# Kernel tuning notes

Measured on AMD Instinct MI355X. Metric: run time of the kernel, lower is better.

## Reference

```python
import jax, jax.numpy as jnp
import numpy as np

NE = 200000   # num_entities
NR = 16       # num_relations
D  = 128      # embed_dim
B  = 4096     # batch
S  = 64       # neighbors per node
L  = 2        # num_layers
H  = 4        # attention heads (hardcoded in module)


def _ln(x, g, b, eps=1e-5):
    m = jnp.mean(x, -1, keepdims=True)
    v = jnp.mean((x - m) ** 2, -1, keepdims=True)
    return (x - m) * jax.lax.rsqrt(v + eps) * g + b


def setup_inputs() -> dict:
    key = jax.random.key(0)
    ks = jax.random.split(key, 12)
    s = 0.05
    return {
        'drug_entity_indices': jax.random.randint(ks[0], (B,), 0, NE),
        'adj_entity': jax.random.randint(ks[1], (B, S), 0, NE),
        'adj_relation': jax.random.randint(ks[2], (B, S), 0, NR),
        'edge_weights': jax.random.uniform(ks[3], (B, S), dtype=jnp.float32),
        'entity_emb': jax.random.normal(ks[4], (NE, D), jnp.float32) * s,
        'W_rgcn': jax.random.normal(ks[5], (L, NR, D, D), jnp.float32) * s,
        'res_w': jax.random.normal(ks[6], (L, D, D), jnp.float32) * s,
        'res_b': jnp.zeros((L, D), jnp.float32),
        'proj_w': jax.random.normal(ks[7], (L, D, D), jnp.float32) * s,
        'proj_b': jnp.zeros((L, D), jnp.float32),
        'ln_g': jnp.ones((L, D), jnp.float32),
        'ln_b': jnp.zeros((L, D), jnp.float32),
        'in_proj_w': jax.random.normal(ks[8], (3 * D, D), jnp.float32) * s,
        'in_proj_b': jnp.zeros((3 * D,), jnp.float32),
        'out_proj_w': jax.random.normal(ks[9], (D, D), jnp.float32) * s,
        'out_proj_b': jnp.zeros((D,), jnp.float32),
        'fln_g': jnp.ones((D,), jnp.float32),
        'fln_b': jnp.zeros((D,), jnp.float32),
    }


def reference(drug_entity_indices, adj_entity, adj_relation, edge_weights,
              entity_emb, W_rgcn, res_w, res_b, proj_w, proj_b, ln_g, ln_b,
              in_proj_w, in_proj_b, out_proj_w, out_proj_b, fln_g, fln_b):
    node = entity_emb[drug_entity_indices]           # [B,D] combined_emb
    nbr = entity_emb[adj_entity]                     # [B,S,D]
    # Route each edge to its relation: sum_s nbr*ew*[rel==r] then one GEMM per relation
    # (mathematically identical to the per-relation masked matmul loop in torch).
    onehot = jax.nn.one_hot(adj_relation, NR, dtype=node.dtype)      # [B,S,R]
    pre = jnp.einsum('bsd,bsr->brd', nbr * edge_weights[..., None], onehot)
    outs = []
    for l in range(L):
        msgs = jnp.einsum('brd,rde->be', pre, W_rgcn[l])             # [B,D]
        h = jax.nn.relu(node + msgs + node @ res_w[l].T + res_b[l])  # RGCNAggregator
        node = _ln(h @ proj_w[l].T + proj_b[l] + node, ln_g[l], ln_b[l])
        outs.append(node)
    x = jnp.stack(outs, 0)                           # [L,B,D] seq-first
    qkv = x @ in_proj_w.T + in_proj_b
    q, k, v = jnp.split(qkv, 3, axis=-1)
    hd = D // H
    def heads(t):
        return t.reshape(L, B, H, hd).transpose(1, 2, 0, 3)          # [B,H,L,hd]
    q, k, v = heads(q), heads(k), heads(v)
    att = jax.nn.softmax(jnp.einsum('bhld,bhmd->bhlm', q, k) / np.sqrt(hd).astype(np.float32), axis=-1)
    o = jnp.einsum('bhlm,bhmd->bhld', att, v).transpose(2, 0, 1, 3).reshape(L, B, D)
    o = o @ out_proj_w.T + out_proj_b
    return _ln(o.mean(0), fln_g, fln_b)              # [B,D]
```

## Files before the change

### kernel.cpp

```cpp
#include <hip/hip_runtime.h>
#include <math.h>

#define NRREL 16
#define DDIM 128
#define BBATCH 4096
#define SNBR 64

typedef __attribute__((ext_vector_type(8))) short short8;
typedef __attribute__((ext_vector_type(4))) float floatx4;

__device__ __forceinline__ unsigned short f2bf(float f) {
    unsigned u = __builtin_bit_cast(unsigned, f);
    u += 0x7fffu + ((u >> 16) & 1u);
    return (unsigned short)(u >> 16);
}
__device__ __forceinline__ float bf2f(unsigned short u) {
    return __builtin_bit_cast(float, ((unsigned)u) << 16);
}

__device__ __forceinline__ void gl_lds16(const unsigned short* g, unsigned short* l) {
    __builtin_amdgcn_global_load_lds(
        (const __attribute__((address_space(1))) void*)g,
        (__attribute__((address_space(3))) void*)l, 16, 0, 0);
}

extern "C" __global__ __launch_bounds__(256)
void k_front(const int* __restrict__ drug, const int* __restrict__ adj_e,
             const int* __restrict__ adj_r, const float* __restrict__ ew,
             const float* __restrict__ emb, const float* __restrict__ W_rgcn,
             const float* __restrict__ res_w, const float* __restrict__ proj_w,
             const float* __restrict__ in_w, const float* __restrict__ out_w,
             unsigned short* __restrict__ pre_bf, float* __restrict__ node_f,
             unsigned short* __restrict__ Wcat, unsigned short* __restrict__ resw,
             unsigned short* __restrict__ projw, unsigned short* __restrict__ inw,
             unsigned short* __restrict__ outw)
{
    __shared__ union {
        struct {
            int memb[16][64];
            int cnt[16];
            int sent[64];
            float swt[64];
        } g;
        struct { float tileT[64 * 65]; } w;
    } sm;

    const int bid = blockIdx.x, t = threadIdx.x;

    if (bid < BBATCH) {
        const int b = bid;
        if (t < 16) sm.g.cnt[t] = 0;
        __syncthreads();
        if (t < 64) {
            sm.g.sent[t] = adj_e[b * SNBR + t];
            sm.g.swt[t]  = ew[b * SNBR + t];
            int r = adj_r[b * SNBR + t];
            int slot = atomicAdd(&sm.g.cnt[r], 1);
            sm.g.memb[r][slot] = t;
        }
        if (t >= 64 && t < 96) {
            int tt = t - 64;
            float4 nf = *(const float4*)(emb + (size_t)drug[b] * DDIM + 4 * tt);
            *(float4*)(node_f + (size_t)b * DDIM + 4 * tt) = nf;
        }
        __syncthreads();
        const int r = t >> 4, g8 = t & 15;
        const int n = sm.g.cnt[r];
        float acc[8] = {0.f, 0.f, 0.f, 0.f, 0.f, 0.f, 0.f, 0.f};
        if (n > 0) {
            int s = sm.g.memb[r][0];
            float wq = sm.g.swt[s];
            const float* p = emb + (size_t)sm.g.sent[s] * DDIM + 8 * g8;
            float4 v0 = *(const float4*)p;
            float4 v1 = *(const float4*)(p + 4);
            for (int j = 1; j < n; ++j) {
                int s2 = sm.g.memb[r][j];
                float wq2 = sm.g.swt[s2];
                const float* p2 = emb + (size_t)sm.g.sent[s2] * DDIM + 8 * g8;
                float4 u0 = *(const float4*)p2;
                float4 u1 = *(const float4*)(p2 + 4);
                acc[0] = fmaf(v0.x, wq, acc[0]); acc[1] = fmaf(v0.y, wq, acc[1]);
                acc[2] = fmaf(v0.z, wq, acc[2]); acc[3] = fmaf(v0.w, wq, acc[3]);
                acc[4] = fmaf(v1.x, wq, acc[4]); acc[5] = fmaf(v1.y, wq, acc[5]);
                acc[6] = fmaf(v1.z, wq, acc[6]); acc[7] = fmaf(v1.w, wq, acc[7]);
                v0 = u0; v1 = u1; wq = wq2;
            }
            acc[0] = fmaf(v0.x, wq, acc[0]); acc[1] = fmaf(v0.y, wq, acc[1]);
            acc[2] = fmaf(v0.z, wq, acc[2]); acc[3] = fmaf(v0.w, wq, acc[3]);
            acc[4] = fmaf(v1.x, wq, acc[4]); acc[5] = fmaf(v1.y, wq, acc[5]);
            acc[6] = fmaf(v1.z, wq, acc[6]); acc[7] = fmaf(v1.w, wq, acc[7]);
        }
        short8 o;
        #pragma unroll
        for (int jj = 0; jj < 8; ++jj) o[jj] = (short)f2bf(acc[jj]);
        *(short8*)(pre_bf + (size_t)b * 2048 + r * DDIM + 8 * g8) = o;
    } else if (bid < BBATCH + 128) {
        const int bid2 = bid - BBATCH;
        const int l = bid2 >> 6, rem = bid2 & 63;
        const int k0 = (rem >> 1) * 64, e0 = (rem & 1) * 64;
        #pragma unroll
        for (int i = 0; i < 4; ++i) {
            int flat = t + 256 * i;
            int k = flat >> 4, c = flat & 15;
            float4 v = *(const float4*)(W_rgcn + ((size_t)(l * 2048 + k0 + k)) * 128 + e0 + 4 * c);
            sm.w.tileT[(4 * c + 0) * 65 + k] = v.x;
            sm.w.tileT[(4 * c + 1) * 65 + k] = v.y;
            sm.w.tileT[(4 * c + 2) * 65 + k] = v.z;
            sm.w.tileT[(4 * c + 3) * 65 + k] = v.w;
        }
        __syncthreads();
        const int e = t >> 2, m = t & 3;
        #pragma unroll
        for (int half = 0; half < 2; ++half) {
            int kk = 16 * m + 8 * half;
            short8 o;
            #pragma unroll
            for (int j = 0; j < 8; ++j) o[j] = (short)f2bf(sm.w.tileT[e * 65 + kk + j]);
            *(short8*)(Wcat + ((size_t)(l * 128 + e0 + e)) * 2048 + k0 + kk) = o;
        }
    } else {
        int j4 = ((bid - BBATCH - 128) * 256 + t) * 4;
        const float* src; unsigned short* dst; int off;
        if (j4 < 32768)       { src = res_w;  dst = resw;  off = j4; }
        else if (j4 < 65536)  { src = proj_w; dst = projw; off = j4 - 32768; }
        else if (j4 < 114688) { src = in_w;   dst = inw;   off = j4 - 65536; }
        else                  { src = out_w;  dst = outw;  off = j4 - 114688; }
        float4 v = *(const float4*)(src + off);
        ushort4 o = { f2bf(v.x), f2bf(v.y), f2bf(v.z), f2bf(v.w) };
        *(ushort4*)(dst + off) = o;
    }
}

extern "C" __global__ __launch_bounds__(512)
void k_tail(const unsigned short* __restrict__ pre_bf, const unsigned short* __restrict__ Wcat,
            const float* __restrict__ node_fg,
            const unsigned short* __restrict__ resw, const unsigned short* __restrict__ projw,
            const float* __restrict__ res_b, const float* __restrict__ proj_b,
            const float* __restrict__ ln_g, const float* __restrict__ ln_b,
            const unsigned short* __restrict__ inw, const float* __restrict__ in_b,
            const unsigned short* __restrict__ outw, const float* __restrict__ out_b,
            const float* __restrict__ fg, const float* __restrict__ fb,
            float* __restrict__ outp)
{
    __shared__ union {
        struct { unsigned short preA[16 * 2056]; } a;
        struct {
            unsigned short h_b16[16 * 136];
            unsigned short xs_l[32 * 136];
            unsigned short qkvl[32 * 392];
        } t;
    } sm;
    __shared__ float node_ln[16 * 132];
    __shared__ unsigned short node_b16[16 * 136];
    __shared__ float msum[16 * 260];
    __shared__ float psum[8][16], psq[8][16];

    const int t = threadIdx.x, w = t >> 6, lane = t & 63, l15 = lane & 15, q = lane >> 4;
    const int r0 = blockIdx.x * 16;

    #pragma unroll
    for (int i = 0; i < 8; ++i) {
        int row = 2 * w + (i & 1), chunk = i >> 1;
        gl_lds16(pre_bf + (size_t)(r0 + row) * 2048 + chunk * 512 + 8 * lane,
                 sm.a.preA + row * 2056 + chunk * 512);
    }
    {
        int rr = t >> 5, c = t & 31;
        float4 v = *(const float4*)(node_fg + (size_t)(r0 + rr) * DDIM + 4 * c);
        *(float4*)(node_ln + rr * 132 + 4 * c) = v;
        ushort4 o = { f2bf(v.x), f2bf(v.y), f2bf(v.z), f2bf(v.w) };
        *(ushort4*)(node_b16 + rr * 136 + 4 * c) = o;
    }
    __syncthreads();

    {
        floatx4 macc[2] = {};
        const unsigned short* ap = sm.a.preA + l15 * 2056 + 8 * q;
        const unsigned short* bp = Wcat + (size_t)(32 * w + l15) * 2048 + 8 * q;
        #pragma unroll 8
        for (int k = 0; k < 2048; k += 32) {
            short8 A = *(const short8*)(ap + k);
            #pragma unroll
            for (int ni = 0; ni < 2; ++ni) {
                short8 B = *(const short8*)(bp + (size_t)(ni * 16) * 2048 + k);
                macc[ni] = __builtin_amdgcn_mfma_f32_16x16x32_bf16(A, B, macc[ni], 0, 0, 0);
            }
        }
        #pragma unroll
        for (int ni = 0; ni < 2; ++ni) {
            int gc = 32 * w + ni * 16 + l15;
            #pragma unroll
            for (int r = 0; r < 4; ++r)
                msum[(4 * q + r) * 260 + gc] = macc[ni][r];
        }
    }
    __syncthreads();

    for (int l = 0; l < 2; ++l) {
        {
            const unsigned short* Bw = resw + (size_t)l * DDIM * DDIM;
            floatx4 acc = {};
            const unsigned short* ap = node_b16 + l15 * 136 + 8 * q;
            #pragma unroll
            for (int kk = 0; kk < DDIM; kk += 32) {
                short8 A = *(const short8*)(ap + kk);
                short8 B = *(const short8*)(Bw + (size_t)(16 * w + l15) * DDIM + kk + 8 * q);
                acc = __builtin_amdgcn_mfma_f32_16x16x32_bf16(A, B, acc, 0, 0, 0);
            }
            int gc = 16 * w + l15;
            float rb = res_b[l * DDIM + gc];
            #pragma unroll
            for (int r = 0; r < 4; ++r) {
                int lr = 4 * q + r;
                float v = acc[r] + rb + node_ln[lr * 132 + gc] + msum[lr * 260 + l * DDIM + gc];
                sm.t.h_b16[lr * 136 + gc] = f2bf(v > 0.f ? v : 0.f);
            }
        }
        __syncthreads();
        {
            const unsigned short* Bw = projw + (size_t)l * DDIM * DDIM;
            floatx4 acc = {};
            const unsigned short* ap = sm.t.h_b16 + l15 * 136 + 8 * q;
            #pragma unroll
            for (int kk = 0; kk < DDIM; kk += 32) {
                short8 A = *(const short8*)(ap + kk);
                short8 B = *(const short8*)(Bw + (size_t)(16 * w + l15) * DDIM + kk + 8 * q);
                acc = __builtin_amdgcn_mfma_f32_16x16x32_bf16(A, B, acc, 0, 0, 0);
            }
            int gc = 16 * w + l15;
            float vv[4];
            float s4[4] = {0, 0, 0, 0}, sq4[4] = {0, 0, 0, 0};
            float pb = proj_b[l * DDIM + gc];
            #pragma unroll
            for (int r = 0; r < 4; ++r) {
                int lr = 4 * q + r;
                float v = acc[r] + pb + node_ln[lr * 132 + gc];
                vv[r] = v; s4[r] += v; sq4[r] += v * v;
            }
            #pragma unroll
            for (int r = 0; r < 4; ++r)
                #pragma unroll
                for (int off2 = 8; off2 >= 1; off2 >>= 1) {
                    s4[r] += __shfl_xor(s4[r], off2, 64);
                    sq4[r] += __shfl_xor(sq4[r], off2, 64);
                }
            if (l15 == 0) {
                #pragma unroll
                for (int r = 0; r < 4; ++r) {
                    psum[w][4 * q + r] = s4[r];
                    psq[w][4 * q + r] = sq4[r];
                }
            }
            __syncthreads();
            float g2 = ln_g[l * DDIM + gc], bb = ln_b[l * DDIM + gc];
            #pragma unroll
            for (int r = 0; r < 4; ++r) {
                int lr = 4 * q + r;
                float ssum = 0.f, ssq = 0.f;
                #pragma unroll
                for (int ww = 0; ww < 8; ++ww) { ssum += psum[ww][lr]; ssq += psq[ww][lr]; }
                float mean = ssum * (1.f / DDIM);
                float var = ssq * (1.f / DDIM) - mean * mean;
                float val = (vv[r] - mean) * rsqrtf(var + 1e-5f) * g2 + bb;
                node_ln[lr * 132 + gc] = val;
                unsigned short ub = f2bf(val);
                node_b16[lr * 136 + gc] = ub;
                sm.t.xs_l[(2 * lr + l) * 136 + gc] = ub;
            }
            __syncthreads();
        }
    }

    {
        floatx4 acc[6] = {};
        const unsigned short* ap = sm.t.xs_l + (16 * (w & 1) + l15) * 136 + 8 * q;
        #pragma unroll
        for (int kk = 0; kk < DDIM; kk += 32) {
            short8 A = *(const short8*)(ap + kk);
            #pragma unroll
            for (int ni = 0; ni < 6; ++ni) {
                short8 B = *(const short8*)(inw + (size_t)(96 * (w >> 1) + ni * 16 + l15) * DDIM + kk + 8 * q);
                acc[ni] = __builtin_amdgcn_mfma_f32_16x16x32_bf16(A, B, acc[ni], 0, 0, 0);
            }
        }
        #pragma unroll
        for (int ni = 0; ni < 6; ++ni) {
            int gc = 96 * (w >> 1) + ni * 16 + l15;
            float ib = in_b[gc];
            #pragma unroll
            for (int r = 0; r < 4; ++r)
                sm.t.qkvl[(16 * (w & 1) + 4 * q + r) * 392 + gc] = f2bf(acc[ni][r] + ib);
        }
    }
    __syncthreads();

    if (t < 128) {
        int g4 = t >> 3, j = t & 7;
        const unsigned short* row0 = sm.t.qkvl + (2 * g4) * 392;
        const unsigned short* row1 = row0 + 392;
        float p00 = 0.f, p01 = 0.f, p10 = 0.f, p11 = 0.f;
        #pragma unroll
        for (int dd = 0; dd < 16; ++dd) {
            int d = 16 * j + dd;
            float q0 = bf2f(row0[d]), k0 = bf2f(row0[128 + d]);
            float q1 = bf2f(row1[d]), k1 = bf2f(row1[128 + d]);
            p00 = fmaf(q0, k0, p00); p01 = fmaf(q0, k1, p01);
            p10 = fmaf(q1, k0, p10); p11 = fmaf(q1, k1, p11);
        }
        p00 += __shfl_xor(p00, 1, 64); p01 += __shfl_xor(p01, 1, 64);
        p10 += __shfl_xor(p10, 1, 64); p11 += __shfl_xor(p11, 1, 64);
        const float sc = 0.17677669529663687f;
        p00 *= sc; p01 *= sc; p10 *= sc; p11 *= sc;
        float m0 = fmaxf(p00, p01), e00 = expf(p00 - m0), e01 = expf(p01 - m0);
        float i0 = 1.f / (e00 + e01);
        float m1 = fmaxf(p10, p11), e10 = expf(p10 - m1), e11 = expf(p11 - m1);
        float i1 = 1.f / (e10 + e11);
        #pragma unroll
        for (int dd = 0; dd < 16; ++dd) {
            int d = 16 * j + dd;
            float v0 = bf2f(row0[256 + d]), v1 = bf2f(row1[256 + d]);
            sm.t.xs_l[(2 * g4) * 136 + d]     = f2bf((e00 * v0 + e01 * v1) * i0);
            sm.t.xs_l[(2 * g4 + 1) * 136 + d] = f2bf((e10 * v0 + e11 * v1) * i1);
        }
    }
    __syncthreads();

    {
        floatx4 acc[2] = {};
        const unsigned short* ap = sm.t.xs_l + (16 * (w & 1) + l15) * 136 + 8 * q;
        #pragma unroll
        for (int kk = 0; kk < DDIM; kk += 32) {
            short8 A = *(const short8*)(ap + kk);
            #pragma unroll
            for (int ni = 0; ni < 2; ++ni) {
                short8 B = *(const short8*)(outw + (size_t)(32 * (w >> 1) + ni * 16 + l15) * DDIM + kk + 8 * q);
                acc[ni] = __builtin_amdgcn_mfma_f32_16x16x32_bf16(A, B, acc[ni], 0, 0, 0);
            }
        }
        float av[2][2];
        float s2[2] = {0, 0}, sq2[2] = {0, 0};
        #pragma unroll
        for (int ni = 0; ni < 2; ++ni) {
            int gc = 32 * (w >> 1) + ni * 16 + l15;
            float ob = out_b[gc];
            #pragma unroll
            for (int rr = 0; rr < 2; ++rr) {
                float v = 0.5f * (acc[ni][2 * rr] + acc[ni][2 * rr + 1]) + ob;
                av[ni][rr] = v; s2[rr] += v; sq2[rr] += v * v;
            }
        }
        #pragma unroll
        for (int rr = 0; rr < 2; ++rr)
            #pragma unroll
            for (int off2 = 8; off2 >= 1; off2 >>= 1) {
                s2[rr] += __shfl_xor(s2[rr], off2, 64);
                sq2[rr] += __shfl_xor(sq2[rr], off2, 64);
            }
        if (l15 == 0) {
            #pragma unroll
            for (int rr = 0; rr < 2; ++rr) {
                psum[w][2 * q + rr] = s2[rr];
                psq[w][2 * q + rr] = sq2[rr];
            }
        }
        __syncthreads();
        #pragma unroll
        for (int ni = 0; ni < 2; ++ni) {
            int gc = 32 * (w >> 1) + ni * 16 + l15;
            float g2 = fg[gc], bb = fb[gc];
            #pragma unroll
            for (int rr = 0; rr < 2; ++rr) {
                int idx = 2 * q + rr;
                int bl = 8 * (w & 1) + idx;
                float ssum = psum[w & 1][idx] + psum[(w & 1) + 2][idx]
                           + psum[(w & 1) + 4][idx] + psum[(w & 1) + 6][idx];
                float ssq  = psq[w & 1][idx] + psq[(w & 1) + 2][idx]
                           + psq[(w & 1) + 4][idx] + psq[(w & 1) + 6][idx];
                float mean = ssum * (1.f / DDIM);
                float var = ssq * (1.f / DDIM) - mean * mean;
                outp[(size_t)(r0 + bl) * DDIM + gc] = (av[ni][rr] - mean) * rsqrtf(var + 1e-5f) * g2 + bb;
            }
        }
    }
}

extern "C" void kernel_launch(void* const* d_in, const int* in_sizes, int n_in,
                              void* d_out, int out_size, void* d_ws, size_t ws_size,
                              hipStream_t stream) {
    const int*   drug_idx = (const int*)d_in[0];
    const int*   adj_ent  = (const int*)d_in[1];
    const int*   adj_rel  = (const int*)d_in[2];
    const float* ew       = (const float*)d_in[3];
    const float* emb      = (const float*)d_in[4];
    const float* W_rgcn   = (const float*)d_in[5];
    const float* res_w    = (const float*)d_in[6];
    const float* res_b    = (const float*)d_in[7];
    const float* proj_w   = (const float*)d_in[8];
    const float* proj_b   = (const float*)d_in[9];
    const float* ln_g     = (const float*)d_in[10];
    const float* ln_b     = (const float*)d_in[11];
    const float* in_w     = (const float*)d_in[12];
    const float* in_b     = (const float*)d_in[13];
    const float* out_w    = (const float*)d_in[14];
    const float* out_b    = (const float*)d_in[15];
    const float* fg       = (const float*)d_in[16];
    const float* fb       = (const float*)d_in[17];
    float* outp = (float*)d_out;

    char* ws = (char*)d_ws;
    size_t off = 0;
    auto alloc = [&](size_t bytes) { size_t o = off; off = (off + bytes + 255) & ~(size_t)255; return o; };
    unsigned short* pre_bf  = (unsigned short*)(ws + alloc((size_t)BBATCH * 2048 * 2));
    float*          node_f  = (float*)         (ws + alloc((size_t)BBATCH * 128 * 4));
    unsigned short* Wcat    = (unsigned short*)(ws + alloc((size_t)256 * 2048 * 2));
    unsigned short* resw    = (unsigned short*)(ws + alloc((size_t)2 * 128 * 128 * 2));
    unsigned short* projw   = (unsigned short*)(ws + alloc((size_t)2 * 128 * 128 * 2));
    unsigned short* inw     = (unsigned short*)(ws + alloc((size_t)384 * 128 * 2));
    unsigned short* outw    = (unsigned short*)(ws + alloc((size_t)128 * 128 * 2));

    hipLaunchKernelGGL(k_front, dim3(BBATCH + 256), dim3(256), 0, stream,
                       drug_idx, adj_ent, adj_rel, ew, emb, W_rgcn,
                       res_w, proj_w, in_w, out_w,
                       pre_bf, node_f, Wcat, resw, projw, inw, outw);
    hipLaunchKernelGGL(k_tail, dim3(256), dim3(512), 0, stream,
                       pre_bf, Wcat, node_f, resw, projw, res_b, proj_b, ln_g, ln_b,
                       inw, in_b, outw, out_b, fg, fb, outp);
}
```

Measured before the change: 240.6 us.

## Fuse neighbor gather and relation binning into the tail kernel

Moves the per-relation weighted neighbor aggregation from the front kernel into the main tail kernel, which now writes pre-activations straight into LDS. This removes the bf16 pre buffer (16 MB) and node buffer round trip through global memory. The front kernel keeps only weight conversion. The gather now runs on only 256 blocks instead of 4096, which lowers the parallelism available to hide the latency of the random embedding loads.

```diff
diff --git a/kernel.cpp b/kernel.cpp
--- a/kernel.cpp
+++ b/kernel.cpp
@@ -18,95 +18,29 @@
     return __builtin_bit_cast(float, ((unsigned)u) << 16);
 }
 
-__device__ __forceinline__ void gl_lds16(const unsigned short* g, unsigned short* l) {
-    __builtin_amdgcn_global_load_lds(
-        (const __attribute__((address_space(1))) void*)g,
-        (__attribute__((address_space(3))) void*)l, 16, 0, 0);
-}
-
 extern "C" __global__ __launch_bounds__(256)
-void k_front(const int* __restrict__ drug, const int* __restrict__ adj_e,
-             const int* __restrict__ adj_r, const float* __restrict__ ew,
-             const float* __restrict__ emb, const float* __restrict__ W_rgcn,
-             const float* __restrict__ res_w, const float* __restrict__ proj_w,
-             const float* __restrict__ in_w, const float* __restrict__ out_w,
-             unsigned short* __restrict__ pre_bf, float* __restrict__ node_f,
-             unsigned short* __restrict__ Wcat, unsigned short* __restrict__ resw,
-             unsigned short* __restrict__ projw, unsigned short* __restrict__ inw,
-             unsigned short* __restrict__ outw)
+void k_prep(const float* __restrict__ W_rgcn,
+            const float* __restrict__ res_w, const float* __restrict__ proj_w,
+            const float* __restrict__ in_w, const float* __restrict__ out_w,
+            unsigned short* __restrict__ Wcat, unsigned short* __restrict__ resw,
+            unsigned short* __restrict__ projw, unsigned short* __restrict__ inw,
+            unsigned short* __restrict__ outw)
 {
-    __shared__ union {
-        struct {
-            int memb[16][64];
-            int cnt[16];
-            int sent[64];
-            float swt[64];
-        } g;
-        struct { float tileT[64 * 65]; } w;
-    } sm;
-
+    __shared__ float tileT[64 * 65];
     const int bid = blockIdx.x, t = threadIdx.x;
 
-    if (bid < BBATCH) {
-        const int b = bid;
-        if (t < 16) sm.g.cnt[t] = 0;
-        __syncthreads();
-        if (t < 64) {
-            sm.g.sent[t] = adj_e[b * SNBR + t];
-            sm.g.swt[t]  = ew[b * SNBR + t];
-            int r = adj_r[b * SNBR + t];
-            int slot = atomicAdd(&sm.g.cnt[r], 1);
-            sm.g.memb[r][slot] = t;
-        }
-        if (t >= 64 && t < 96) {
-            int tt = t - 64;
-            float4 nf = *(const float4*)(emb + (size_t)drug[b] * DDIM + 4 * tt);
-            *(float4*)(node_f + (size_t)b * DDIM + 4 * tt) = nf;
-        }
-        __syncthreads();
-        const int r = t >> 4, g8 = t & 15;
-        const int n = sm.g.cnt[r];
-        float acc[8] = {0.f, 0.f, 0.f, 0.f, 0.f, 0.f, 0.f, 0.f};
-        if (n > 0) {
-            int s = sm.g.memb[r][0];
-            float wq = sm.g.swt[s];
-            const float* p = emb + (size_t)sm.g.sent[s] * DDIM + 8 * g8;
-            float4 v0 = *(const float4*)p;
-            float4 v1 = *(const float4*)(p + 4);
-            for (int j = 1; j < n; ++j) {
-                int s2 = sm.g.memb[r][j];
-                float wq2 = sm.g.swt[s2];
-                const float* p2 = emb + (size_t)sm.g.sent[s2] * DDIM + 8 * g8;
-                float4 u0 = *(const float4*)p2;
-                float4 u1 = *(const float4*)(p2 + 4);
-                acc[0] = fmaf(v0.x, wq, acc[0]); acc[1] = fmaf(v0.y, wq, acc[1]);
-                acc[2] = fmaf(v0.z, wq, acc[2]); acc[3] = fmaf(v0.w, wq, acc[3]);
-                acc[4] = fmaf(v1.x, wq, acc[4]); acc[5] = fmaf(v1.y, wq, acc[5]);
-                acc[6] = fmaf(v1.z, wq, acc[6]); acc[7] = fmaf(v1.w, wq, acc[7]);
-                v0 = u0; v1 = u1; wq = wq2;
-            }
-            acc[0] = fmaf(v0.x, wq, acc[0]); acc[1] = fmaf(v0.y, wq, acc[1]);
-            acc[2] = fmaf(v0.z, wq, acc[2]); acc[3] = fmaf(v0.w, wq, acc[3]);
-            acc[4] = fmaf(v1.x, wq, acc[4]); acc[5] = fmaf(v1.y, wq, acc[5]);
-            acc[6] = fmaf(v1.z, wq, acc[6]); acc[7] = fmaf(v1.w, wq, acc[7]);
-        }
-        short8 o;
-        #pragma unroll
-        for (int jj = 0; jj < 8; ++jj) o[jj] = (short)f2bf(acc[jj]);
-        *(short8*)(pre_bf + (size_t)b * 2048 + r * DDIM + 8 * g8) = o;
-    } else if (bid < BBATCH + 128) {
-        const int bid2 = bid - BBATCH;
-        const int l = bid2 >> 6, rem = bid2 & 63;
+    if (bid < 128) {
+        const int l = bid >> 6, rem = bid & 63;
         const int k0 = (rem >> 1) * 64, e0 = (rem & 1) * 64;
         #pragma unroll
         for (int i = 0; i < 4; ++i) {
             int flat = t + 256 * i;
             int k = flat >> 4, c = flat & 15;
             float4 v = *(const float4*)(W_rgcn + ((size_t)(l * 2048 + k0 + k)) * 128 + e0 + 4 * c);
-            sm.w.tileT[(4 * c + 0) * 65 + k] = v.x;
-            sm.w.tileT[(4 * c + 1) * 65 + k] = v.y;
-            sm.w.tileT[(4 * c + 2) * 65 + k] = v.z;
-            sm.w.tileT[(4 * c + 3) * 65 + k] = v.w;
+            tileT[(4 * c + 0) * 65 + k] = v.x;
+            tileT[(4 * c + 1) * 65 + k] = v.y;
+            tileT[(4 * c + 2) * 65 + k] = v.z;
+            tileT[(4 * c + 3) * 65 + k] = v.w;
         }
         __syncthreads();
         const int e = t >> 2, m = t & 3;
@@ -115,11 +49,11 @@
             int kk = 16 * m + 8 * half;
             short8 o;
             #pragma unroll
-            for (int j = 0; j < 8; ++j) o[j] = (short)f2bf(sm.w.tileT[e * 65 + kk + j]);
+            for (int j = 0; j < 8; ++j) o[j] = (short)f2bf(tileT[e * 65 + kk + j]);
             *(short8*)(Wcat + ((size_t)(l * 128 + e0 + e)) * 2048 + k0 + kk) = o;
         }
     } else {
-        int j4 = ((bid - BBATCH - 128) * 256 + t) * 4;
+        int j4 = ((bid - 128) * 256 + t) * 4;
         const float* src; unsigned short* dst; int off;
         if (j4 < 32768)       { src = res_w;  dst = resw;  off = j4; }
         else if (j4 < 65536)  { src = proj_w; dst = projw; off = j4 - 32768; }
@@ -132,15 +66,17 @@
 }
 
 extern "C" __global__ __launch_bounds__(512)
-void k_tail(const unsigned short* __restrict__ pre_bf, const unsigned short* __restrict__ Wcat,
-            const float* __restrict__ node_fg,
-            const unsigned short* __restrict__ resw, const unsigned short* __restrict__ projw,
-            const float* __restrict__ res_b, const float* __restrict__ proj_b,
-            const float* __restrict__ ln_g, const float* __restrict__ ln_b,
-            const unsigned short* __restrict__ inw, const float* __restrict__ in_b,
-            const unsigned short* __restrict__ outw, const float* __restrict__ out_b,
-            const float* __restrict__ fg, const float* __restrict__ fb,
-            float* __restrict__ outp)
+void k_fused(const int* __restrict__ drug, const int* __restrict__ adj_e,
+             const int* __restrict__ adj_r, const float* __restrict__ ew,
+             const float* __restrict__ emb,
+             const unsigned short* __restrict__ Wcat,
+             const unsigned short* __restrict__ resw, const unsigned short* __restrict__ projw,
+             const float* __restrict__ res_b, const float* __restrict__ proj_b,
+             const float* __restrict__ ln_g, const float* __restrict__ ln_b,
+             const unsigned short* __restrict__ inw, const float* __restrict__ in_b,
+             const unsigned short* __restrict__ outw, const float* __restrict__ out_b,
+             const float* __restrict__ fg, const float* __restrict__ fb,
+             float* __restrict__ outp)
 {
     __shared__ union {
         struct { unsigned short preA[16 * 2056]; } a;
@@ -152,24 +88,103 @@
     } sm;
     __shared__ float node_ln[16 * 132];
     __shared__ unsigned short node_b16[16 * 136];
-    __shared__ float msum[16 * 260];
+    __shared__ union {
+        struct {
+            int   sent[16][64];
+            float swt[16][64];
+            int   cnt[16][16];
+            int   strt[16][16];
+            unsigned char memb[16][64];
+            unsigned char rel[16][64];
+        } g;
+        float msum[16 * 260];
+    } sg;
     __shared__ float psum[8][16], psq[8][16];
 
     const int t = threadIdx.x, w = t >> 6, lane = t & 63, l15 = lane & 15, q = lane >> 4;
     const int r0 = blockIdx.x * 16;
 
     #pragma unroll
-    for (int i = 0; i < 8; ++i) {
-        int row = 2 * w + (i & 1), chunk = i >> 1;
-        gl_lds16(pre_bf + (size_t)(r0 + row) * 2048 + chunk * 512 + 8 * lane,
-                 sm.a.preA + row * 2056 + chunk * 512);
-    }
+    for (int i = 0; i < 2; ++i) {
+        int f = t + 512 * i;
+        int row = f >> 6, s = f & 63;
+        sg.g.sent[row][s] = adj_e[(r0 + row) * SNBR + s];
+        sg.g.swt[row][s]  = ew[(r0 + row) * SNBR + s];
+        sg.g.rel[row][s]  = (unsigned char)adj_r[(r0 + row) * SNBR + s];
+    }
+    if (t < 256) sg.g.cnt[t >> 4][t & 15] = 0;
     {
         int rr = t >> 5, c = t & 31;
-        float4 v = *(const float4*)(node_fg + (size_t)(r0 + rr) * DDIM + 4 * c);
+        int di = drug[r0 + rr];
+        float4 v = *(const float4*)(emb + (size_t)di * DDIM + 4 * c);
         *(float4*)(node_ln + rr * 132 + 4 * c) = v;
         ushort4 o = { f2bf(v.x), f2bf(v.y), f2bf(v.z), f2bf(v.w) };
         *(ushort4*)(node_b16 + rr * 136 + 4 * c) = o;
+    }
+    __syncthreads();
+
+    #pragma unroll
+    for (int i = 0; i < 2; ++i) {
+        int f = t + 512 * i;
+        int row = f >> 6, s = f & 63;
+        atomicAdd(&sg.g.cnt[row][sg.g.rel[row][s]], 1);
+    }
+    __syncthreads();
+
+    if (t < 16) {
+        int a = 0;
+        #pragma unroll
+        for (int r = 0; r < NRREL; ++r) { sg.g.strt[t][r] = a; a += sg.g.cnt[t][r]; }
+    }
+    __syncthreads();
+
+    #pragma unroll
+    for (int i = 0; i < 2; ++i) {
+        int f = t + 512 * i;
+        int row = f >> 6, s = f & 63;
+        int pos = atomicAdd(&sg.g.strt[row][sg.g.rel[row][s]], 1);
+        sg.g.memb[row][pos] = (unsigned char)s;
+    }
+    __syncthreads();
+
+    {
+        const int h = t >> 8, tt = t & 255;
+        const int rl = tt >> 4, g8 = tt & 15;
+        #pragma unroll 1
+        for (int p = 0; p < 8; ++p) {
+            int row = 2 * p + h;
+            int n = sg.g.cnt[row][rl];
+            int end = sg.g.strt[row][rl];
+            int beg = end - n;
+            float acc[8] = {0.f, 0.f, 0.f, 0.f, 0.f, 0.f, 0.f, 0.f};
+            if (n > 0) {
+                int s = sg.g.memb[row][beg];
+                float wq = sg.g.swt[row][s];
+                const float* pp = emb + (size_t)sg.g.sent[row][s] * DDIM + 8 * g8;
+                float4 v0 = *(const float4*)pp;
+                float4 v1 = *(const float4*)(pp + 4);
+                for (int j = beg + 1; j < end; ++j) {
+                    int s2 = sg.g.memb[row][j];
+                    float w2 = sg.g.swt[row][s2];
+                    const float* p2 = emb + (size_t)sg.g.sent[row][s2] * DDIM + 8 * g8;
+                    float4 u0 = *(const float4*)p2;
+                    float4 u1 = *(const float4*)(p2 + 4);
+                    acc[0] = fmaf(v0.x, wq, acc[0]); acc[1] = fmaf(v0.y, wq, acc[1]);
+                    acc[2] = fmaf(v0.z, wq, acc[2]); acc[3] = fmaf(v0.w, wq, acc[3]);
+                    acc[4] = fmaf(v1.x, wq, acc[4]); acc[5] = fmaf(v1.y, wq, acc[5]);
+                    acc[6] = fmaf(v1.z, wq, acc[6]); acc[7] = fmaf(v1.w, wq, acc[7]);
+                    v0 = u0; v1 = u1; wq = w2;
+                }
+                acc[0] = fmaf(v0.x, wq, acc[0]); acc[1] = fmaf(v0.y, wq, acc[1]);
+                acc[2] = fmaf(v0.z, wq, acc[2]); acc[3] = fmaf(v0.w, wq, acc[3]);
+                acc[4] = fmaf(v1.x, wq, acc[4]); acc[5] = fmaf(v1.y, wq, acc[5]);
+                acc[6] = fmaf(v1.z, wq, acc[6]); acc[7] = fmaf(v1.w, wq, acc[7]);
+            }
+            short8 o;
+            #pragma unroll
+            for (int jj = 0; jj < 8; ++jj) o[jj] = (short)f2bf(acc[jj]);
+            *(short8*)(sm.a.preA + row * 2056 + rl * DDIM + 8 * g8) = o;
+        }
     }
     __syncthreads();
 
@@ -191,7 +206,7 @@
             int gc = 32 * w + ni * 16 + l15;
             #pragma unroll
             for (int r = 0; r < 4; ++r)
-                msum[(4 * q + r) * 260 + gc] = macc[ni][r];
+                sg.msum[(4 * q + r) * 260 + gc] = macc[ni][r];
         }
     }
     __syncthreads();
@@ -212,7 +227,7 @@
             #pragma unroll
             for (int r = 0; r < 4; ++r) {
                 int lr = 4 * q + r;
-                float v = acc[r] + rb + node_ln[lr * 132 + gc] + msum[lr * 260 + l * DDIM + gc];
+                float v = acc[r] + rb + node_ln[lr * 132 + gc] + sg.msum[lr * 260 + l * DDIM + gc];
                 sm.t.h_b16[lr * 136 + gc] = f2bf(v > 0.f ? v : 0.f);
             }
         }
@@ -410,19 +425,17 @@
     char* ws = (char*)d_ws;
     size_t off = 0;
     auto alloc = [&](size_t bytes) { size_t o = off; off = (off + bytes + 255) & ~(size_t)255; return o; };
-    unsigned short* pre_bf  = (unsigned short*)(ws + alloc((size_t)BBATCH * 2048 * 2));
-    float*          node_f  = (float*)         (ws + alloc((size_t)BBATCH * 128 * 4));
     unsigned short* Wcat    = (unsigned short*)(ws + alloc((size_t)256 * 2048 * 2));
     unsigned short* resw    = (unsigned short*)(ws + alloc((size_t)2 * 128 * 128 * 2));
     unsigned short* projw   = (unsigned short*)(ws + alloc((size_t)2 * 128 * 128 * 2));
     unsigned short* inw     = (unsigned short*)(ws + alloc((size_t)384 * 128 * 2));
     unsigned short* outw    = (unsigned short*)(ws + alloc((size_t)128 * 128 * 2));
 
-    hipLaunchKernelGGL(k_front, dim3(BBATCH + 256), dim3(256), 0, stream,
-                       drug_idx, adj_ent, adj_rel, ew, emb, W_rgcn,
-                       res_w, proj_w, in_w, out_w,
-                       pre_bf, node_f, Wcat, resw, projw, inw, outw);
-    hipLaunchKernelGGL(k_tail, dim3(256), dim3(512), 0, stream,
-                       pre_bf, Wcat, node_f, resw, projw, res_b, proj_b, ln_g, ln_b,
+    hipLaunchKernelGGL(k_prep, dim3(256), dim3(256), 0, stream,
+                       W_rgcn, res_w, proj_w, in_w, out_w,
+                       Wcat, resw, projw, inw, outw);
+    hipLaunchKernelGGL(k_fused, dim3(256), dim3(512), 0, stream,
+                       drug_idx, adj_ent, adj_rel, ew, emb,
+                       Wcat, resw, projw, res_b, proj_b, ln_g, ln_b,
                        inw, in_b, outw, out_b, fg, fb, outp);
 }
```

New measurement: 245.2 us. Within noise of the previous version (+1.9%).
